# Performance work log

Hardware: AMD Instinct MI355X
Metric: run time of the kernel (lower is better)

The kernel has to match this reference:

```python
import jax, jax.numpy as jnp
import numpy as np

N_NODES = 50000
N_EDGES = 1250000
HID = 64
N_LAYERS = 3
N_GRAPHS = 64
EPS = 1e-5


def setup_inputs() -> dict:
    key = jax.random.key(0)
    ks = jax.random.split(key, 12)
    x = jnp.arange(N_NODES, dtype=jnp.int64) if jax.config.jax_enable_x64 else jnp.arange(N_NODES, dtype=jnp.int32)
    edge_index = jax.random.randint(ks[0], (2, N_EDGES), 0, N_NODES)
    edge_weight = jax.random.uniform(ks[1], (N_EDGES,), dtype=jnp.float32)
    batch = jnp.sort(jax.random.randint(ks[2], (N_NODES,), 0, N_GRAPHS))
    # parameters
    emb = 0.02 * jax.random.normal(ks[3], (N_NODES, HID), dtype=jnp.float32)
    def xavier(k, shape):
        fan_in, fan_out = shape[-2], shape[-1]
        lim = np.sqrt(6.0 / (fan_in + fan_out))
        return jax.random.uniform(k, shape, jnp.float32, -lim, lim)
    convW = xavier(ks[4], (N_LAYERS, HID, HID))
    convB = jnp.zeros((N_LAYERS, HID), jnp.float32)
    lnG = jnp.ones((N_LAYERS, HID), jnp.float32)
    lnB = jnp.zeros((N_LAYERS, HID), jnp.float32)
    W1 = xavier(ks[5], (2 * HID, HID))
    b1 = jnp.zeros((HID,), jnp.float32)
    W2 = xavier(ks[6], (HID, 1))
    b2 = jnp.zeros((1,), jnp.float32)
    return {"x": x, "edge_index": edge_index, "edge_weight": edge_weight, "batch": batch,
            "emb": emb, "convW": convW, "convB": convB, "lnG": lnG, "lnB": lnB,
            "W1": W1, "b1": b1, "W2": W2, "b2": b2}


def _layernorm(h, g, b):
    mu = jnp.mean(h, axis=-1, keepdims=True)
    var = jnp.mean((h - mu) ** 2, axis=-1, keepdims=True)
    return (h - mu) * jax.lax.rsqrt(var + EPS) * g + b


def reference(x, edge_index, edge_weight, batch, emb, convW, convB, lnG, lnB, W1, b1, W2, b2):
    src, dst = edge_index[0], edge_index[1]
    h = emb[x]  # [N, H]
    n = h.shape[0]
    for i in range(N_LAYERS):
        m = h @ convW[i]                                   # linear transform
        msg = m[src] * edge_weight[:, None]                # gather + edge weighting
        h = jax.ops.segment_sum(msg, dst, num_segments=n)  # scatter-add aggregate
        h = h + convB[i]
        h = jax.nn.relu(_layernorm(h, lnG[i], lnB[i]))
    # pooling per graph
    counts = jax.ops.segment_sum(jnp.ones((n,), h.dtype), batch, num_segments=N_GRAPHS)
    mean_x = jax.ops.segment_sum(h, batch, num_segments=N_GRAPHS) / jnp.maximum(counts, 1.0)[:, None]
    max_x = jax.ops.segment_max(h, batch, num_segments=N_GRAPHS)
    max_x = jnp.where(counts[:, None] > 0, max_x, 0.0)
    g = jnp.concatenate([mean_x, max_x], axis=1)           # [G, 2H]
    g = jax.nn.relu(g @ W1 + b1)
    out = g @ W2 + b2
    return out.squeeze(-1)
```

## Files before the change

kernel.cpp:

```cpp
#include <hip/hip_runtime.h>
#include <hip/hip_fp16.h>

#define N_NODES 50000
#define N_EDGES 1250000
#define HID 64
#define N_LAYERS 3
#define N_GRAPHS 64
#define EPS 1e-5f

#define P_SHIFT 7
#define P_NODES 128
#define NP ((N_NODES + P_NODES - 1) / P_NODES)
#define PCAP 4096

#define LB_NODES 8

__device__ inline float2 up2(unsigned u) {
    __half2 h;
    *reinterpret_cast<unsigned*>(&h) = u;
    return __half22float2(h);
}
__device__ inline unsigned pk2(float a, float b) {
    __half2 h = __floats2half2_rn(a, b);
    return *reinterpret_cast<unsigned*>(&h);
}

__global__ __launch_bounds__(256) void k_embed(const int* __restrict__ x,
                                               const float4* __restrict__ emb4,
                                               uint4* __restrict__ h8) {
    int i = blockIdx.x * 256 + threadIdx.x;
    if (i < N_NODES * 8) {
        int row = i >> 3, q = i & 7;
        float4 fa = emb4[x[row] * 16 + q * 2];
        float4 fb = emb4[x[row] * 16 + q * 2 + 1];
        uint4 u;
        u.x = pk2(fa.x, fa.y); u.y = pk2(fa.z, fa.w);
        u.z = pk2(fb.x, fb.y); u.w = pk2(fb.z, fb.w);
        h8[i] = u;
    }
}

__global__ __launch_bounds__(1024) void k_part(const int* __restrict__ src,
                                               const int* __restrict__ dst,
                                               const float* __restrict__ w,
                                               int* __restrict__ pcnt,
                                               int2* __restrict__ part) {
    __shared__ int hist[NP];
    __shared__ int cur[NP];
    int t = threadIdx.x;
    for (int k = t; k < NP; k += 1024) { hist[k] = 0; cur[k] = 0; }
    __syncthreads();
    int chunk = (N_EDGES + gridDim.x - 1) / gridDim.x;
    int e0 = blockIdx.x * chunk;
    int e1 = min(e0 + chunk, N_EDGES);
    for (int e = e0 + t; e < e1; e += 1024)
        atomicAdd(&hist[dst[e] >> P_SHIFT], 1);
    __syncthreads();
    for (int k = t; k < NP; k += 1024) {
        int c = hist[k];
        hist[k] = c ? atomicAdd(&pcnt[k], c) : 0;
    }
    __syncthreads();
    for (int e = e0 + t; e < e1; e += 1024) {
        int d = dst[e];
        int b = d >> P_SHIFT;
        int r = atomicAdd(&cur[b], 1);
        part[(b << 12) + hist[b] + r] =
            make_int2(((d & (P_NODES - 1)) << 16) | src[e], __float_as_int(w[e]));
    }
}

__global__ __launch_bounds__(512) void k_sort(const int2* __restrict__ part,
                                              const int* __restrict__ pcnt,
                                              unsigned* __restrict__ csr16,
                                              int* __restrict__ rowbeg,
                                              int* __restrict__ rowend,
                                              const int* __restrict__ batch,
                                              int* __restrict__ start,
                                              float* __restrict__ sums,
                                              unsigned* __restrict__ maxs) {
    __shared__ int2 sbuf[PCAP];
    __shared__ int cnt[P_NODES], base[P_NODES], cur[P_NODES];
    int p = blockIdx.x, t = threadIdx.x;
    if (t < P_NODES) cnt[t] = 0;
    __syncthreads();
    int n = pcnt[p];
    if (n > PCAP) n = PCAP;
    const int2* pb = part + (p << 12);
    for (int i = t; i < n; i += 512) atomicAdd(&cnt[pb[i].x >> 16], 1);
    __syncthreads();
    if (t < P_NODES) base[t] = cnt[t];
    __syncthreads();
    for (int off = 1; off < P_NODES; off <<= 1) {
        int v = (t < P_NODES && t >= off) ? base[t - off] : 0;
        __syncthreads();
        if (t < P_NODES) base[t] += v;
        __syncthreads();
    }
    if (t < P_NODES) cur[t] = base[t] - cnt[t];
    __syncthreads();
    for (int i = t; i < n; i += 512) {
        int2 e = pb[i];
        int pos = atomicAdd(&cur[e.x >> 16], 1);
        sbuf[pos] = e;
    }
    __syncthreads();
    for (int i = t; i < n; i += 512) {
        int2 e = sbuf[i];
        unsigned short wb = __half_as_ushort(__float2half_rn(__int_as_float(e.y)));
        csr16[(p << 12) + i] = (unsigned)(e.x & 0xFFFF) | ((unsigned)wb << 16);
    }
    if (t < P_NODES) {
        int node = p * P_NODES + t;
        if (node < N_NODES) {
            rowbeg[node] = (p << 12) + base[t] - cnt[t];
            rowend[node] = (p << 12) + base[t];
        }
    }
    if (p == 0) {
        if (t <= N_GRAPHS) {
            int lo = 0, hi = N_NODES;
            while (lo < hi) {
                int mid = (lo + hi) >> 1;
                if (batch[mid] < t) lo = mid + 1; else hi = mid;
            }
            start[t] = lo;
        }
        for (int k = t; k < N_GRAPHS * HID; k += 512) {
            sums[k] = 0.f;
            maxs[k] = 0u;
        }
    }
}

__global__ __launch_bounds__(512) void k_layer(const uint4* __restrict__ h8,
                                               const int* __restrict__ rowbeg,
                                               const int* __restrict__ rowend,
                                               const unsigned* __restrict__ csr16,
                                               const float* __restrict__ W,
                                               const float* __restrict__ bias,
                                               const float* __restrict__ g,
                                               const float* __restrict__ b,
                                               unsigned short* __restrict__ hout) {
    __shared__ float Wl[HID * HID];
    __shared__ float aggl[LB_NODES][HID];
    int tid = threadIdx.x;
    for (int k = tid; k < HID * HID; k += 512) Wl[k] = W[k];
    __syncthreads();
    int wv = tid >> 6, lane = tid & 63;
    int grp = lane >> 3, c8 = lane & 7;
    int row = blockIdx.x * LB_NODES + wv;
    int p0 = __builtin_amdgcn_readfirstlane(rowbeg[row]);
    int p1 = __builtin_amdgcn_readfirstlane(rowend[row]);
    int last = p1 - 1;
    float A0[8], A1[8], A2[8], A3[8];
#pragma unroll
    for (int q = 0; q < 8; ++q) { A0[q] = 0.f; A1[q] = 0.f; A2[q] = 0.f; A3[q] = 0.f; }
    for (int p = p0; p <= last; p += 32) {
        int i0 = p + grp, i1 = i0 + 8, i2 = i0 + 16, i3 = i0 + 24;
        unsigned e0 = csr16[min(i0, last)];
        unsigned e1 = csr16[min(i1, last)];
        unsigned e2 = csr16[min(i2, last)];
        unsigned e3 = csr16[min(i3, last)];
        float w0 = (i0 <= last) ? __half2float(__ushort_as_half((unsigned short)(e0 >> 16))) : 0.f;
        float w1 = (i1 <= last) ? __half2float(__ushort_as_half((unsigned short)(e1 >> 16))) : 0.f;
        float w2 = (i2 <= last) ? __half2float(__ushort_as_half((unsigned short)(e2 >> 16))) : 0.f;
        float w3 = (i3 <= last) ? __half2float(__ushort_as_half((unsigned short)(e3 >> 16))) : 0.f;
        uint4 v0 = h8[(e0 & 0xFFFF) * 8 + c8];
        uint4 v1 = h8[(e1 & 0xFFFF) * 8 + c8];
        uint4 v2 = h8[(e2 & 0xFFFF) * 8 + c8];
        uint4 v3 = h8[(e3 & 0xFFFF) * 8 + c8];
        float2 f;
        f = up2(v0.x); A0[0] += f.x * w0; A0[1] += f.y * w0;
        f = up2(v0.y); A0[2] += f.x * w0; A0[3] += f.y * w0;
        f = up2(v0.z); A0[4] += f.x * w0; A0[5] += f.y * w0;
        f = up2(v0.w); A0[6] += f.x * w0; A0[7] += f.y * w0;
        f = up2(v1.x); A1[0] += f.x * w1; A1[1] += f.y * w1;
        f = up2(v1.y); A1[2] += f.x * w1; A1[3] += f.y * w1;
        f = up2(v1.z); A1[4] += f.x * w1; A1[5] += f.y * w1;
        f = up2(v1.w); A1[6] += f.x * w1; A1[7] += f.y * w1;
        f = up2(v2.x); A2[0] += f.x * w2; A2[1] += f.y * w2;
        f = up2(v2.y); A2[2] += f.x * w2; A2[3] += f.y * w2;
        f = up2(v2.z); A2[4] += f.x * w2; A2[5] += f.y * w2;
        f = up2(v2.w); A2[6] += f.x * w2; A2[7] += f.y * w2;
        f = up2(v3.x); A3[0] += f.x * w3; A3[1] += f.y * w3;
        f = up2(v3.y); A3[2] += f.x * w3; A3[3] += f.y * w3;
        f = up2(v3.z); A3[4] += f.x * w3; A3[5] += f.y * w3;
        f = up2(v3.w); A3[6] += f.x * w3; A3[7] += f.y * w3;
    }
    float acc[8];
#pragma unroll
    for (int q = 0; q < 8; ++q) {
        float s = (A0[q] + A1[q]) + (A2[q] + A3[q]);
        s += __shfl_xor(s, 8, 64);
        s += __shfl_xor(s, 16, 64);
        s += __shfl_xor(s, 32, 64);
        acc[q] = s;
    }
    if (grp == 0) {
#pragma unroll
        for (int q = 0; q < 8; ++q) aggl[wv][c8 * 8 + q] = acc[q];
    }
    const float* agg = &aggl[wv][0];
    int j = lane;
    float mv = 0.f;
#pragma unroll 16
    for (int k = 0; k < HID; ++k) mv += agg[k] * Wl[k * HID + j];
    float v = mv + bias[j];
    float s = v;
#pragma unroll
    for (int off = 32; off; off >>= 1) s += __shfl_xor(s, off, 64);
    float mu = s * (1.f / 64.f);
    float d = v - mu;
    float vv = d * d;
#pragma unroll
    for (int off = 32; off; off >>= 1) vv += __shfl_xor(vv, off, 64);
    float var = vv * (1.f / 64.f);
    float y = fmaxf(d * rsqrtf(var + EPS) * g[j] + b[j], 0.f);
    hout[row * HID + j] = __half_as_ushort(__float2half_rn(y));
}

#define NSLICE 16
__global__ __launch_bounds__(256) void k_pool2(const unsigned short* __restrict__ h,
                                               const int* __restrict__ start,
                                               float* __restrict__ sums,
                                               unsigned* __restrict__ maxs) {
    int gph = blockIdx.x >> 4;
    int sl  = blockIdx.x & (NSLICE - 1);
    int s = start[gph], e1 = start[gph + 1];
    int len = e1 - s;
    int chunk = (len + NSLICE - 1) / NSLICE;
    int r0 = s + sl * chunk;
    int r1 = min(r0 + chunk, e1);
    int j = threadIdx.x & 63, wv = threadIdx.x >> 6;
    float sm = 0.f, mx = 0.f;
    for (int r = r0 + wv; r < r1; r += 4) {
        float v = __half2float(__ushort_as_half(h[r * HID + j]));
        sm += v;
        mx = fmaxf(mx, v);
    }
    atomicAdd(&sums[gph * HID + j], sm);
    atomicMax(&maxs[gph * HID + j], __float_as_uint(mx));
}

__global__ __launch_bounds__(64) void k_mlp(const float* __restrict__ sums,
                                            const unsigned* __restrict__ maxs,
                                            const int* __restrict__ start,
                                            const float* __restrict__ W1,
                                            const float* __restrict__ b1,
                                            const float* __restrict__ W2,
                                            const float* __restrict__ b2,
                                            float* __restrict__ out) {
    int gph = blockIdx.x;
    int j = threadIdx.x;
    __shared__ float gv[2 * HID];
    int cnt = start[gph + 1] - start[gph];
    float inv = 1.f / fmaxf((float)cnt, 1.f);
    gv[j] = sums[gph * HID + j] * inv;
    float mx = __uint_as_float(maxs[gph * HID + j]);
    gv[HID + j] = (cnt > 0) ? mx : 0.f;
    __syncthreads();
    float acc = b1[j];
#pragma unroll
    for (int k = 0; k < 2 * HID; ++k) acc += gv[k] * W1[k * HID + j];
    acc = fmaxf(acc, 0.f);
    float p = acc * W2[j];
#pragma unroll
    for (int off = 32; off; off >>= 1) p += __shfl_xor(p, off, 64);
    if (j == 0) out[gph] = p + b2[0];
}

extern "C" void kernel_launch(void* const* d_in, const int* in_sizes, int n_in,
                              void* d_out, int out_size, void* d_ws, size_t ws_size,
                              hipStream_t stream) {
    const int*   x     = (const int*)d_in[0];
    const int*   ei    = (const int*)d_in[1];
    const float* ew    = (const float*)d_in[2];
    const int*   batch = (const int*)d_in[3];
    const float* emb   = (const float*)d_in[4];
    const float* convW = (const float*)d_in[5];
    const float* convB = (const float*)d_in[6];
    const float* lnG   = (const float*)d_in[7];
    const float* lnB   = (const float*)d_in[8];
    const float* W1    = (const float*)d_in[9];
    const float* b1    = (const float*)d_in[10];
    const float* W2    = (const float*)d_in[11];
    const float* b2    = (const float*)d_in[12];
    float* out = (float*)d_out;

    unsigned short* hA = (unsigned short*)d_ws;
    unsigned short* hB = hA + (size_t)N_NODES * HID;
    int2*  part   = (int2*)(hB + (size_t)N_NODES * HID);
    unsigned* csr16 = (unsigned*)(part + (size_t)NP * PCAP);
    int*   pcnt   = (int*)(csr16 + (size_t)NP * PCAP);
    int*   rowbeg = pcnt + NP;
    int*   rowend = rowbeg + N_NODES;
    float* sums   = (float*)(rowend + N_NODES);
    unsigned* maxs = (unsigned*)(sums + N_GRAPHS * HID);
    int*   start  = (int*)(maxs + N_GRAPHS * HID);

    const int* src = ei;
    const int* dst = ei + N_EDGES;

    hipMemsetAsync(pcnt, 0, NP * sizeof(int), stream);
    k_part<<<256, 1024, 0, stream>>>(src, dst, ew, pcnt, part);
    k_sort<<<NP, 512, 0, stream>>>(part, pcnt, csr16, rowbeg, rowend,
                                   batch, start, sums, maxs);
    k_embed<<<(N_NODES * 8 + 255) / 256, 256, 0, stream>>>(
        x, (const float4*)emb, (uint4*)hA);

    unsigned short* bufs[2] = { hA, hB };
    for (int L = 0; L < N_LAYERS; ++L) {
        k_layer<<<N_NODES / LB_NODES, 512, 0, stream>>>(
            (const uint4*)bufs[L & 1], rowbeg, rowend, csr16,
            convW + L * HID * HID, convB + L * HID,
            lnG + L * HID, lnB + L * HID, bufs[(L + 1) & 1]);
    }
    const unsigned short* hfin = bufs[N_LAYERS & 1];

    k_pool2<<<N_GRAPHS * NSLICE, 256, 0, stream>>>(hfin, start, sums, maxs);
    k_mlp<<<N_GRAPHS, 64, 0, stream>>>(sums, maxs, start, W1, b1, W2, b2, out);
}
```

Measured before the change: 289.1 us.

## Split layer into gather kernel and MFMA-based transform with fused LayerNorm

The fused per-layer kernel is split into two kernels. The first only aggregates neighbor features and writes them as fp16. The second loads 64-row tiles and does the 64x64 weight multiply with 16x16x16 fp16 MFMA instructions, then applies bias, LayerNorm and ReLU. This removes the per-block weight load into shared memory and the scalar dot-product loop from the gather kernel. In exchange it adds an extra fp16 round trip of the aggregate through global memory, an extra launch per layer, and rounds the aggregate and weights to fp16.

```diff
diff --git a/kernel.cpp b/kernel.cpp
--- a/kernel.cpp
+++ b/kernel.cpp
@@ -13,7 +13,8 @@
 #define NP ((N_NODES + P_NODES - 1) / P_NODES)
 #define PCAP 4096
 
-#define LB_NODES 8
+typedef _Float16 half4f __attribute__((ext_vector_type(4)));
+typedef float f32x4 __attribute__((ext_vector_type(4)));
 
 __device__ inline float2 up2(unsigned u) {
     __half2 h;
@@ -133,23 +134,15 @@
     }
 }
 
-__global__ __launch_bounds__(512) void k_layer(const uint4* __restrict__ h8,
-                                               const int* __restrict__ rowbeg,
-                                               const int* __restrict__ rowend,
-                                               const unsigned* __restrict__ csr16,
-                                               const float* __restrict__ W,
-                                               const float* __restrict__ bias,
-                                               const float* __restrict__ g,
-                                               const float* __restrict__ b,
-                                               unsigned short* __restrict__ hout) {
-    __shared__ float Wl[HID * HID];
-    __shared__ float aggl[LB_NODES][HID];
+__global__ __launch_bounds__(512) void k_gather(const uint4* __restrict__ h8,
+                                                const int* __restrict__ rowbeg,
+                                                const int* __restrict__ rowend,
+                                                const unsigned* __restrict__ csr16,
+                                                uint4* __restrict__ agg8) {
     int tid = threadIdx.x;
-    for (int k = tid; k < HID * HID; k += 512) Wl[k] = W[k];
-    __syncthreads();
     int wv = tid >> 6, lane = tid & 63;
     int grp = lane >> 3, c8 = lane & 7;
-    int row = blockIdx.x * LB_NODES + wv;
+    int row = blockIdx.x * 8 + wv;
     int p0 = __builtin_amdgcn_readfirstlane(rowbeg[row]);
     int p1 = __builtin_amdgcn_readfirstlane(rowend[row]);
     int last = p1 - 1;
@@ -198,26 +191,110 @@
         acc[q] = s;
     }
     if (grp == 0) {
-#pragma unroll
-        for (int q = 0; q < 8; ++q) aggl[wv][c8 * 8 + q] = acc[q];
-    }
-    const float* agg = &aggl[wv][0];
-    int j = lane;
-    float mv = 0.f;
-#pragma unroll 16
-    for (int k = 0; k < HID; ++k) mv += agg[k] * Wl[k * HID + j];
-    float v = mv + bias[j];
-    float s = v;
-#pragma unroll
-    for (int off = 32; off; off >>= 1) s += __shfl_xor(s, off, 64);
-    float mu = s * (1.f / 64.f);
-    float d = v - mu;
-    float vv = d * d;
-#pragma unroll
-    for (int off = 32; off; off >>= 1) vv += __shfl_xor(vv, off, 64);
-    float var = vv * (1.f / 64.f);
-    float y = fmaxf(d * rsqrtf(var + EPS) * g[j] + b[j], 0.f);
-    hout[row * HID + j] = __half_as_ushort(__float2half_rn(y));
+        uint4 u;
+        u.x = pk2(acc[0], acc[1]); u.y = pk2(acc[2], acc[3]);
+        u.z = pk2(acc[4], acc[5]); u.w = pk2(acc[6], acc[7]);
+        agg8[row * 8 + c8] = u;
+    }
+}
+
+#define APITCH 68
+__global__ __launch_bounds__(256) void k_xform(const uint4* __restrict__ agg8,
+                                               const float* __restrict__ W,
+                                               const float* __restrict__ bias,
+                                               const float* __restrict__ gam,
+                                               const float* __restrict__ bet,
+                                               uint4* __restrict__ hout8) {
+    __shared__ _Float16 Al[64][APITCH];
+    __shared__ _Float16 Cl[64][APITCH];
+    __shared__ float Wl[HID * HID];
+    __shared__ float prm[3 * HID];
+    int tid = threadIdx.x;
+    int row0 = blockIdx.x * 64;
+    for (int idx = tid; idx < 512; idx += 256) {
+        int r = idx >> 3, c8 = idx & 7;
+        uint4 u = make_uint4(0u, 0u, 0u, 0u);
+        if (row0 + r < N_NODES) u = agg8[(row0 + r) * 8 + c8];
+        unsigned* dstp = (unsigned*)&Al[r][c8 * 8];
+        dstp[0] = u.x; dstp[1] = u.y; dstp[2] = u.z; dstp[3] = u.w;
+    }
+    for (int idx = tid; idx < HID * HID; idx += 256) Wl[idx] = W[idx];
+    if (tid < HID) {
+        prm[tid] = bias[tid];
+        prm[HID + tid] = gam[tid];
+        prm[2 * HID + tid] = bet[tid];
+    }
+    __syncthreads();
+    int wv = tid >> 6, lane = tid & 63;
+    int g4 = lane >> 4, l15 = lane & 15;
+    f32x4 acc[4] = {f32x4{0,0,0,0}, f32x4{0,0,0,0}, f32x4{0,0,0,0}, f32x4{0,0,0,0}};
+#pragma unroll
+    for (int kc = 0; kc < 4; ++kc) {
+        half4f a = *(const half4f*)&Al[wv * 16 + l15][kc * 16 + g4 * 4];
+        int kb = kc * 16 + g4 * 4;
+#pragma unroll
+        for (int ct = 0; ct < 4; ++ct) {
+            int cb = ct * 16 + l15;
+            half4f bf;
+            bf[0] = (_Float16)Wl[(kb + 0) * HID + cb];
+            bf[1] = (_Float16)Wl[(kb + 1) * HID + cb];
+            bf[2] = (_Float16)Wl[(kb + 2) * HID + cb];
+            bf[3] = (_Float16)Wl[(kb + 3) * HID + cb];
+            acc[ct] = __builtin_amdgcn_mfma_f32_16x16x16f16(a, bf, acc[ct], 0, 0, 0);
+        }
+    }
+#pragma unroll
+    for (int ct = 0; ct < 4; ++ct) {
+        float bb = prm[ct * 16 + l15];
+#pragma unroll
+        for (int i = 0; i < 4; ++i) acc[ct][i] += bb;
+    }
+    float rs[4];
+#pragma unroll
+    for (int i = 0; i < 4; ++i)
+        rs[i] = (acc[0][i] + acc[1][i]) + (acc[2][i] + acc[3][i]);
+#pragma unroll
+    for (int i = 0; i < 4; ++i) {
+        rs[i] += __shfl_xor(rs[i], 1, 64);
+        rs[i] += __shfl_xor(rs[i], 2, 64);
+        rs[i] += __shfl_xor(rs[i], 4, 64);
+        rs[i] += __shfl_xor(rs[i], 8, 64);
+    }
+    float sq[4];
+#pragma unroll
+    for (int i = 0; i < 4; ++i) {
+        float mu = rs[i] * (1.f / 64.f);
+#pragma unroll
+        for (int ct = 0; ct < 4; ++ct) acc[ct][i] -= mu;
+        sq[i] = (acc[0][i] * acc[0][i] + acc[1][i] * acc[1][i])
+              + (acc[2][i] * acc[2][i] + acc[3][i] * acc[3][i]);
+    }
+#pragma unroll
+    for (int i = 0; i < 4; ++i) {
+        sq[i] += __shfl_xor(sq[i], 1, 64);
+        sq[i] += __shfl_xor(sq[i], 2, 64);
+        sq[i] += __shfl_xor(sq[i], 4, 64);
+        sq[i] += __shfl_xor(sq[i], 8, 64);
+    }
+#pragma unroll
+    for (int ct = 0; ct < 4; ++ct) {
+        int col = ct * 16 + l15;
+        float gg = prm[HID + col], bb = prm[2 * HID + col];
+#pragma unroll
+        for (int i = 0; i < 4; ++i) {
+            float scale = rsqrtf(sq[i] * (1.f / 64.f) + EPS);
+            float y = fmaxf(acc[ct][i] * scale * gg + bb, 0.f);
+            Cl[wv * 16 + g4 * 4 + i][col] = (_Float16)y;
+        }
+    }
+    __syncthreads();
+    for (int idx = tid; idx < 512; idx += 256) {
+        int r = idx >> 3, c8 = idx & 7;
+        if (row0 + r < N_NODES) {
+            const unsigned* sp = (const unsigned*)&Cl[r][c8 * 8];
+            hout8[(row0 + r) * 8 + c8] = make_uint4(sp[0], sp[1], sp[2], sp[3]);
+        }
+    }
 }
 
 #define NSLICE 16
@@ -290,7 +367,8 @@
 
     unsigned short* hA = (unsigned short*)d_ws;
     unsigned short* hB = hA + (size_t)N_NODES * HID;
-    int2*  part   = (int2*)(hB + (size_t)N_NODES * HID);
+    unsigned short* agg = hB + (size_t)N_NODES * HID;
+    int2*  part   = (int2*)(agg + (size_t)N_NODES * HID);
     unsigned* csr16 = (unsigned*)(part + (size_t)NP * PCAP);
     int*   pcnt   = (int*)(csr16 + (size_t)NP * PCAP);
     int*   rowbeg = pcnt + NP;
@@ -311,10 +389,11 @@
 
     unsigned short* bufs[2] = { hA, hB };
     for (int L = 0; L < N_LAYERS; ++L) {
-        k_layer<<<N_NODES / LB_NODES, 512, 0, stream>>>(
-            (const uint4*)bufs[L & 1], rowbeg, rowend, csr16,
-            convW + L * HID * HID, convB + L * HID,
-            lnG + L * HID, lnB + L * HID, bufs[(L + 1) & 1]);
+        k_gather<<<N_NODES / 8, 512, 0, stream>>>(
+            (const uint4*)bufs[L & 1], rowbeg, rowend, csr16, (uint4*)agg);
+        k_xform<<<(N_NODES + 63) / 64, 256, 0, stream>>>(
+            (const uint4*)agg, convW + L * HID * HID, convB + L * HID,
+            lnG + L * HID, lnB + L * HID, (uint4*)bufs[(L + 1) & 1]);
     }
     const unsigned short* hfin = bufs[N_LAYERS & 1];
 
```

Result: faster. 239.2 us (-17.3%).
